# Kernel optimization log

Hardware: AMD Instinct MI355X
Metric: run time of the kernel (lower is better)

The kernel has to match this reference:

```python
import jax, jax.numpy as jnp
import numpy as np

N, T, IN_DIM = 5000, 100, 32
FEAT, HID, OUT, HEADS = 64, 64, 8, 4
E = 160000
F_IN = FEAT + OUT  # GATCell input = concat(embedding, theta)


def setup_inputs() -> dict:
    key = jax.random.key(0)
    ks = jax.random.split(key, 16)
    s = 0.05
    d = {}
    d["x"] = jax.random.normal(ks[0], (N, T, IN_DIM), jnp.float32)
    d["edge_index"] = jax.random.randint(ks[1], (2, E), 0, N, dtype=jnp.int32)
    # LSTM params (PyTorch gate order: i, f, g, o)
    d["W_ih"] = jax.random.normal(ks[2], (IN_DIM, 4 * FEAT), jnp.float32) * s
    d["W_hh"] = jax.random.normal(ks[3], (FEAT, 4 * FEAT), jnp.float32) * s
    d["b_ih"] = jax.random.normal(ks[4], (4 * FEAT,), jnp.float32) * s
    d["b_hh"] = jax.random.normal(ks[5], (4 * FEAT,), jnp.float32) * s
    # TransformerConv params (lin_q/k/v with bias, lin_skip with bias; concat=False)
    d["Wq"] = jax.random.normal(ks[6], (F_IN, HEADS * HID), jnp.float32) * s
    d["bq"] = jax.random.normal(ks[7], (HEADS * HID,), jnp.float32) * s
    d["Wk"] = jax.random.normal(ks[8], (F_IN, HEADS * HID), jnp.float32) * s
    d["bk"] = jax.random.normal(ks[9], (HEADS * HID,), jnp.float32) * s
    d["Wv"] = jax.random.normal(ks[10], (F_IN, HEADS * HID), jnp.float32) * s
    d["bv"] = jax.random.normal(ks[11], (HEADS * HID,), jnp.float32) * s
    d["Wskip"] = jax.random.normal(ks[12], (F_IN, HID), jnp.float32) * s
    d["bskip"] = jax.random.normal(ks[13], (HID,), jnp.float32) * s
    # GATCell mlp (bias=False)
    d["Wmlp"] = jax.random.normal(ks[14], (HID, OUT), jnp.float32) * s
    return d


def _lstm(x, W_ih, W_hh, b_ih, b_hh):
    # x: [N, T, IN_DIM] -> embedding [T, N, FEAT]
    xs = jnp.transpose(x, (1, 0, 2))

    def step(carry, xt):
        h, c = carry
        gates = xt @ W_ih + h @ W_hh + (b_ih + b_hh)
        i, f, g, o = jnp.split(gates, 4, axis=-1)
        c = jax.nn.sigmoid(f) * c + jax.nn.sigmoid(i) * jnp.tanh(g)
        h = jax.nn.sigmoid(o) * jnp.tanh(c)
        return (h, c), h

    h0 = jnp.zeros((x.shape[0], FEAT), x.dtype)
    _, hs = jax.lax.scan(step, (h0, h0), xs)
    return hs


def _transformer_conv(h, edge_index, Wq, bq, Wk, bk, Wv, bv, Wskip, bskip):
    # h: [N, F_IN]; edge_index: [2, E] (row 0 = source j, row 1 = target i)
    n = h.shape[0]
    src, dst = edge_index[0], edge_index[1]
    q = (h @ Wq + bq).reshape(n, HEADS, HID)
    k = (h @ Wk + bk).reshape(n, HEADS, HID)
    v = (h @ Wv + bv).reshape(n, HEADS, HID)
    # per-edge attention logits [E, HEADS]
    alpha = jnp.einsum('ehd,ehd->eh', q[dst], k[src]) / jnp.sqrt(jnp.float32(HID))
    # segment softmax over incoming edges of each target node
    m = jax.ops.segment_max(alpha, dst, num_segments=n)
    m = jnp.where(jnp.isfinite(m), m, 0.0)
    ex = jnp.exp(alpha - m[dst])
    denom = jax.ops.segment_sum(ex, dst, num_segments=n)
    w = ex / jnp.maximum(denom[dst], 1e-16)
    agg = jax.ops.segment_sum(w[:, :, None] * v[src], dst, num_segments=n)  # [N,H,D]
    out = agg.mean(axis=1)  # concat=False -> average heads
    return out + h @ Wskip + bskip  # root skip connection


def reference(x, edge_index, W_ih, W_hh, b_ih, b_hh, Wq, bq, Wk, bk, Wv, bv,
              Wskip, bskip, Wmlp):
    emb = _lstm(x, W_ih, W_hh, b_ih, b_hh)  # [T, N, FEAT]
    n = x.shape[0]

    def gat_step(theta, emb_t):
        h_in = jnp.concatenate([emb_t, theta], axis=-1)  # [N, F_IN]
        hid = _transformer_conv(h_in, edge_index, Wq, bq, Wk, bk, Wv, bv,
                                Wskip, bskip)
        theta_new = jnp.tanh(hid) @ Wmlp
        return theta_new, theta_new

    theta0 = jnp.zeros((n, OUT), x.dtype)
    _, thetas = jax.lax.scan(gat_step, theta0, emb)  # [T, N, OUT]
    theta = jnp.transpose(thetas, (1, 0, 2))  # [N, T, OUT]

    alpha_beta = theta[:, :, :-3]
    a_b = jax.nn.sigmoid(theta[:, :, -3:-1])
    a = a_b[:, :, 0:1] * a_b[:, :, 1:]
    b = a_b[:, :, 0:1] - a
    c = jax.nn.softplus(theta[:, :, -1:])
    return jnp.concatenate([alpha_beta, a, b, c], axis=-1)
```

## Files before the change

### kernel.cpp

```cpp
#include <hip/hip_runtime.h>
#include <math.h>

#define NN 5000
#define TT 100
#define IND 32
#define FEATD 64
#define HIDD 64
#define OUTD 8
#define NHEADS 4
#define EE 160000
#define FIN 72
#define NHC 256
#define QKV_B 625
#define LSTM_B 625

typedef float floatx2 __attribute__((ext_vector_type(2)));

__device__ __forceinline__ float fsig(float x){ return 1.f/(1.f+__expf(-x)); }
__device__ __forceinline__ float ftanh(float x){ return 1.f - 2.f/(__expf(2.f*x)+1.f); }
__device__ __forceinline__ float fsoftplus(float x){ return (x>20.f)? x : log1pf(__expf(x)); }

__global__ __launch_bounds__(256) void count_edges(const int* __restrict__ dst,
                                                   int* __restrict__ cnt){
    int e = blockIdx.x*256 + threadIdx.x;
    if (e < EE) atomicAdd(&cnt[dst[e]], 1);
}

#define SCAN_N 5120
__global__ __launch_bounds__(1024) void scan_csr(const int* __restrict__ cnt,
                                                 int* __restrict__ row_ptr,
                                                 int* __restrict__ cursor){
    __shared__ int sa[SCAN_N];
    __shared__ int sb[SCAN_N];
    int tid = threadIdx.x;
    for (int i=tid;i<SCAN_N;i+=1024) sa[i] = (i<NN)?cnt[i]:0;
    __syncthreads();
    int *s=sa, *d=sb;
    for (int off=1; off<SCAN_N; off<<=1){
        for (int i=tid;i<SCAN_N;i+=1024){
            int v = s[i];
            if (i>=off) v += s[i-off];
            d[i] = v;
        }
        __syncthreads();
        int* t=s; s=d; d=t;
    }
    for (int i=tid;i<=NN;i+=1024){
        int excl = (i==0)?0:s[i-1];
        row_ptr[i] = excl;
        if (i<NN) cursor[i] = excl;
    }
}

__global__ __launch_bounds__(256) void fill_edges(const int* __restrict__ src,
                                                  const int* __restrict__ dst,
                                                  int* __restrict__ cursor,
                                                  int* __restrict__ col){
    int e = blockIdx.x*256 + threadIdx.x;
    if (e < EE){
        int dn = dst[e];
        int pos = atomicAdd(&cursor[dn], 1);
        col[pos] = src[e];
    }
}

#define LOADKV(e) (*reinterpret_cast<const uint2*>(kv + (size_t)col[(e)]*512 + lane*8))
__global__ __launch_bounds__(256) void attn_step(
    const float* __restrict__ q,
    const unsigned char* __restrict__ kv,
    const float* __restrict__ sk,
    const int* __restrict__ row_ptr,
    const int* __restrict__ col,
    const float* __restrict__ Wmlp,
    float* __restrict__ theta,
    float* __restrict__ out,
    int ts)
{
    __shared__ float mrg[2][5][64];
    int tid = threadIdx.x;
    int wvid = tid >> 6;
    int lane = tid & 63;
    int ln   = wvid >> 1;
    int half = wvid & 1;
    int n = blockIdx.x*2 + ln;
    int e0 = row_ptr[n], e1 = row_ptr[n+1];
    float4 qv = *reinterpret_cast<const float4*>(q + n*NHC + lane*4);
    qv.x *= 0.125f; qv.y *= 0.125f; qv.z *= 0.125f; qv.w *= 0.125f;

    float denA=0.f, denB=0.f;
    float aA0=0.f, aA1=0.f, aA2=0.f, aA3=0.f;
    float aB0=0.f, aB1=0.f, aB2=0.f, aB3=0.f;

    const uint2 zv = {0u,0u};
    uint2 bA0=zv, bA1=zv, bB0=zv, bB1=zv;
    int base = e0 + half;
    if (base     < e1) bA0 = LOADKV(base);
    if (base + 2 < e1) bB0 = LOADKV(base+2);
    if (base + 4 < e1) bA1 = LOADKV(base+4);
    if (base + 6 < e1) bB1 = LOADKV(base+6);
    for (int e = base; e < e1; e += 4){
        uint2 uA = bA0; bA0 = bA1; bA1 = zv;
        uint2 uB = bB0; bB0 = bB1; bB1 = zv;
        if (e + 8  < e1) bA1 = LOADKV(e+8);
        if (e + 10 < e1) bB1 = LOADKV(e+10);

        floatx2 kA0 = __builtin_amdgcn_cvt_pk_f32_fp8(uA.x, false);
        floatx2 kA1 = __builtin_amdgcn_cvt_pk_f32_fp8(uA.x, true);
        floatx2 kB0 = __builtin_amdgcn_cvt_pk_f32_fp8(uB.x, false);
        floatx2 kB1 = __builtin_amdgcn_cvt_pk_f32_fp8(uB.x, true);
        float pA = qv.x*kA0[0] + qv.y*kA0[1] + qv.z*kA1[0] + qv.w*kA1[1];
        float pB = qv.x*kB0[0] + qv.y*kB0[1] + qv.z*kB1[0] + qv.w*kB1[1];
        pA += __shfl_xor(pA,1); pB += __shfl_xor(pB,1);
        pA += __shfl_xor(pA,2); pB += __shfl_xor(pB,2);
        pA += __shfl_xor(pA,4); pB += __shfl_xor(pB,4);
        pA += __shfl_xor(pA,8); pB += __shfl_xor(pB,8);

        float eA = __expf(pA);
        float eB = __expf((e + 2 < e1) ? pB : -INFINITY);
        floatx2 vA0 = __builtin_amdgcn_cvt_pk_f32_fp8(uA.y, false);
        floatx2 vA1 = __builtin_amdgcn_cvt_pk_f32_fp8(uA.y, true);
        floatx2 vB0 = __builtin_amdgcn_cvt_pk_f32_fp8(uB.y, false);
        floatx2 vB1 = __builtin_amdgcn_cvt_pk_f32_fp8(uB.y, true);
        denA += eA;
        aA0 = fmaf(eA, vA0[0], aA0);
        aA1 = fmaf(eA, vA0[1], aA1);
        aA2 = fmaf(eA, vA1[0], aA2);
        aA3 = fmaf(eA, vA1[1], aA3);
        denB += eB;
        aB0 = fmaf(eB, vB0[0], aB0);
        aB1 = fmaf(eB, vB0[1], aB1);
        aB2 = fmaf(eB, vB1[0], aB2);
        aB3 = fmaf(eB, vB1[1], aB3);
    }
    float denom = denA + denB;
    float ax = aA0 + aB0;
    float ay = aA1 + aB1;
    float az = aA2 + aB2;
    float aw = aA3 + aB3;

    if (half == 1){
        mrg[ln][0][lane]=denom;
        mrg[ln][1][lane]=ax; mrg[ln][2][lane]=ay;
        mrg[ln][3][lane]=az; mrg[ln][4][lane]=aw;
    }
    __syncthreads();
    if (half == 1) return;

    denom += mrg[ln][0][lane];
    ax += mrg[ln][1][lane];
    ay += mrg[ln][2][lane];
    az += mrg[ln][3][lane];
    aw += mrg[ln][4][lane];

    float inv = 1.f / fmaxf(denom, 1e-16f);
    ax *= inv; ay *= inv; az *= inv; aw *= inv;
    ax += __shfl_xor(ax,16); ax += __shfl_xor(ax,32);
    ay += __shfl_xor(ay,16); ay += __shfl_xor(ay,32);
    az += __shfl_xor(az,16); az += __shfl_xor(az,32);
    aw += __shfl_xor(aw,16); aw += __shfl_xor(aw,32);
    int d0 = (lane & 15) * 4;
    float4 skv = *reinterpret_cast<const float4*>(sk + n*64 + d0);
    float t0 = ftanh(0.25f*ax + skv.x);
    float t1 = ftanh(0.25f*ay + skv.y);
    float t2 = ftanh(0.25f*az + skv.z);
    float t3 = ftanh(0.25f*aw + skv.w);
    float p8[8];
    #pragma unroll
    for (int j=0;j<8;j++){
        p8[j] = fmaf(t0, Wmlp[(d0+0)*8+j],
                fmaf(t1, Wmlp[(d0+1)*8+j],
                fmaf(t2, Wmlp[(d0+2)*8+j],
                     t3* Wmlp[(d0+3)*8+j])));
    }
    #pragma unroll
    for (int j=0;j<8;j++){
        p8[j] += __shfl_xor(p8[j],1);
        p8[j] += __shfl_xor(p8[j],2);
        p8[j] += __shfl_xor(p8[j],4);
        p8[j] += __shfl_xor(p8[j],8);
    }
    if (lane == 0){
        float4 t0v = {p8[0],p8[1],p8[2],p8[3]};
        float4 t1v = {p8[4],p8[5],p8[6],p8[7]};
        *reinterpret_cast<float4*>(theta + n*8)     = t0v;
        *reinterpret_cast<float4*>(theta + n*8 + 4) = t1v;
        float ab0 = fsig(p8[5]);
        float ab1 = fsig(p8[6]);
        float a  = ab0*ab1;
        float bb = ab0 - a;
        float cc = fsoftplus(p8[7]);
        float4 o0 = {p8[0],p8[1],p8[2],p8[3]};
        float4 o1 = {p8[4],a,bb,cc};
        float* op = out + ((size_t)n*TT + ts)*8;
        *reinterpret_cast<float4*>(op)     = o0;
        *reinterpret_cast<float4*>(op + 4) = o1;
    }
}

__global__ __launch_bounds__(256) void qkv_lstm_step(
    const float* __restrict__ x,
    const float* __restrict__ W_ih, const float* __restrict__ W_hh,
    const float* __restrict__ b_ih, const float* __restrict__ b_hh,
    float* __restrict__ h0, float* __restrict__ h1,
    float* __restrict__ c,
    const float* __restrict__ theta,
    const float* __restrict__ Wq, const float* __restrict__ bq,
    const float* __restrict__ Wk, const float* __restrict__ bk,
    const float* __restrict__ Wv, const float* __restrict__ bv,
    const float* __restrict__ Wsk, const float* __restrict__ bsk,
    float* __restrict__ q, float* __restrict__ sk,
    unsigned char* __restrict__ kv, int t)
{
    int tid = threadIdx.x;
    if (blockIdx.x < QKV_B){
        if (t < 0) return;
        __shared__ float hin[8][72];
        const float* hread = (t & 1) ? h1 : h0;
        int n0 = blockIdx.x * 8;
        for (int i=tid; i<8*72; i+=256){
            int node = i/72, kk = i%72;
            int n = n0 + node;
            hin[node][kk] = (kk<64) ? hread[n*64+kk] : theta[n*8 + (kk-64)];
        }
        __syncthreads();

        if (tid < 208){
            int c4 = tid*4;
            const float* W; const float* b; int ncol; int cc; int kind;
            if (c4 < 256)      { W=Wq;  b=bq;  ncol=256; cc=c4;     kind=0; }
            else if (c4 < 512) { W=Wk;  b=bk;  ncol=256; cc=c4-256; kind=1; }
            else if (c4 < 768) { W=Wv;  b=bv;  ncol=256; cc=c4-512; kind=2; }
            else               { W=Wsk; b=bsk; ncol=64;  cc=c4-768; kind=3; }
            float acc2[8][4];
            #pragma unroll
            for (int nn=0;nn<8;nn++){
                #pragma unroll
                for (int j=0;j<4;j++) acc2[nn][j]=0.f;
            }
            #pragma unroll 4
            for (int kk=0; kk<FIN; kk++){
                float4 w = *reinterpret_cast<const float4*>(W + kk*ncol + cc);
                #pragma unroll
                for (int nn=0;nn<8;nn++){
                    float xv = hin[nn][kk];
                    acc2[nn][0]=fmaf(xv,w.x,acc2[nn][0]);
                    acc2[nn][1]=fmaf(xv,w.y,acc2[nn][1]);
                    acc2[nn][2]=fmaf(xv,w.z,acc2[nn][2]);
                    acc2[nn][3]=fmaf(xv,w.w,acc2[nn][3]);
                }
            }
            float4 bb = *reinterpret_cast<const float4*>(b + cc);
            #pragma unroll
            for (int nn=0;nn<8;nn++){
                int n = n0 + nn;
                float o0=acc2[nn][0]+bb.x, o1=acc2[nn][1]+bb.y;
                float o2=acc2[nn][2]+bb.z, o3=acc2[nn][3]+bb.w;
                if (kind == 0){
                    float4 o = {o0,o1,o2,o3};
                    *reinterpret_cast<float4*>(q + n*NHC + cc) = o;
                } else if (kind == 3){
                    float4 o = {o0,o1,o2,o3};
                    *reinterpret_cast<float4*>(sk + n*64 + cc) = o;
                } else {
                    int pk = __builtin_amdgcn_cvt_pk_fp8_f32(o0, o1, 0,  false);
                    pk     = __builtin_amdgcn_cvt_pk_fp8_f32(o2, o3, pk, true);
                    int off = n*512 + cc*2 + ((kind==2)?4:0);
                    *reinterpret_cast<unsigned int*>(kv + off) = (unsigned int)pk;
                }
            }
        }
    } else {
        int s = t + 1;
        if (s >= TT) return;
        __shared__ float xh[8][96];
        const float* hread = (s & 1) ? h0 : h1;
        float*       hwrit = (s & 1) ? h1 : h0;
        int n0 = (blockIdx.x - QKV_B) * 8;
        for (int i=tid; i<8*96; i+=256){
            int node = i/96, kk = i%96;
            int n = n0 + node;
            xh[node][kk] = (kk<32) ? x[(n*TT + s)*IND + kk]
                                   : ((s == 0) ? 0.f : hread[n*64 + (kk-32)]);
        }
        __syncthreads();

        int d  = tid & 63;
        int wv = tid >> 6;
        float acc[2][4];
        #pragma unroll
        for (int p=0;p<2;p++){
            #pragma unroll
            for (int g=0;g<4;g++) acc[p][g]=0.f;
        }
        #pragma unroll 8
        for (int kk=0; kk<32; kk++){
            const float* Wr = W_ih + kk*256;
            float w0=Wr[d], w1=Wr[d+64], w2=Wr[d+128], w3=Wr[d+192];
            float x0 = xh[wv][kk], x1 = xh[wv+4][kk];
            acc[0][0]=fmaf(x0,w0,acc[0][0]); acc[0][1]=fmaf(x0,w1,acc[0][1]);
            acc[0][2]=fmaf(x0,w2,acc[0][2]); acc[0][3]=fmaf(x0,w3,acc[0][3]);
            acc[1][0]=fmaf(x1,w0,acc[1][0]); acc[1][1]=fmaf(x1,w1,acc[1][1]);
            acc[1][2]=fmaf(x1,w2,acc[1][2]); acc[1][3]=fmaf(x1,w3,acc[1][3]);
        }
        #pragma unroll 8
        for (int kk=0; kk<64; kk++){
            const float* Wr = W_hh + kk*256;
            float w0=Wr[d], w1=Wr[d+64], w2=Wr[d+128], w3=Wr[d+192];
            float x0 = xh[wv][32+kk], x1 = xh[wv+4][32+kk];
            acc[0][0]=fmaf(x0,w0,acc[0][0]); acc[0][1]=fmaf(x0,w1,acc[0][1]);
            acc[0][2]=fmaf(x0,w2,acc[0][2]); acc[0][3]=fmaf(x0,w3,acc[0][3]);
            acc[1][0]=fmaf(x1,w0,acc[1][0]); acc[1][1]=fmaf(x1,w1,acc[1][1]);
            acc[1][2]=fmaf(x1,w2,acc[1][2]); acc[1][3]=fmaf(x1,w3,acc[1][3]);
        }
        float bi0 = b_ih[d]     + b_hh[d];
        float bi1 = b_ih[d+64]  + b_hh[d+64];
        float bi2 = b_ih[d+128] + b_hh[d+128];
        float bi3 = b_ih[d+192] + b_hh[d+192];
        #pragma unroll
        for (int p=0;p<2;p++){
            int n = n0 + wv + p*4;
            float gi = fsig (acc[p][0] + bi0);
            float gf = fsig (acc[p][1] + bi1);
            float gg = ftanh(acc[p][2] + bi2);
            float go = fsig (acc[p][3] + bi3);
            float cold = (s == 0) ? 0.f : c[n*64 + d];
            float cnew = gf*cold + gi*gg;
            float hnew = go*ftanh(cnew);
            c[n*64 + d] = cnew;
            hwrit[n*64 + d] = hnew;
        }
    }
}

extern "C" void kernel_launch(void* const* d_in, const int* in_sizes, int n_in,
                              void* d_out, int out_size, void* d_ws, size_t ws_size,
                              hipStream_t stream) {
    const float* x     = (const float*)d_in[0];
    const int*   ei    = (const int*)  d_in[1];
    const float* W_ih  = (const float*)d_in[2];
    const float* W_hh  = (const float*)d_in[3];
    const float* b_ih  = (const float*)d_in[4];
    const float* b_hh  = (const float*)d_in[5];
    const float* Wq    = (const float*)d_in[6];
    const float* bq    = (const float*)d_in[7];
    const float* Wk    = (const float*)d_in[8];
    const float* bk    = (const float*)d_in[9];
    const float* Wv    = (const float*)d_in[10];
    const float* bv    = (const float*)d_in[11];
    const float* Wsk   = (const float*)d_in[12];
    const float* bsk   = (const float*)d_in[13];
    const float* Wmlp  = (const float*)d_in[14];
    float* out = (float*)d_out;

    float* f = (float*)d_ws;
    float* h0    = f;
    float* h1    = h0 + NN*64;
    float* c     = h1 + NN*64;
    float* theta = c + NN*64;
    float* q     = theta + NN*8;
    float* skb   = q + NN*NHC;
    unsigned char* kvb = (unsigned char*)(skb + NN*64);
    int* ip      = (int*)(kvb + (size_t)NN*512);
    int* row_ptr = ip;
    int* cnt     = row_ptr + (NN+1);
    int* cursor  = cnt + NN;
    int* colv    = cursor + NN;

    const int* src = ei;
    const int* dst = ei + EE;

    hipMemsetAsync(h0, 0, (size_t)NN*(64+64+64+8)*sizeof(float), stream);
    hipMemsetAsync(cnt, 0, (size_t)NN*sizeof(int), stream);

    count_edges<<<(EE+255)/256, 256, 0, stream>>>(dst, cnt);
    scan_csr<<<1, 1024, 0, stream>>>(cnt, row_ptr, cursor);
    fill_edges<<<(EE+255)/256, 256, 0, stream>>>(src, dst, cursor, colv);

    qkv_lstm_step<<<QKV_B + LSTM_B, 256, 0, stream>>>(
        x, W_ih, W_hh, b_ih, b_hh, h0, h1, c, theta,
        Wq,bq, Wk,bk, Wv,bv, Wsk,bsk, q, skb, kvb, -1);

    for (int t=0; t<TT; t++){
        if (t >= 1)
            attn_step<<<NN/2, 256, 0, stream>>>(q, kvb, skb, row_ptr, colv,
                                                Wmlp, theta, out, t-1);
        qkv_lstm_step<<<QKV_B + LSTM_B, 256, 0, stream>>>(
            x, W_ih, W_hh, b_ih, b_hh, h0, h1, c, theta,
            Wq,bq, Wk,bk, Wv,bv, Wsk,bsk, q, skb, kvb, t);
    }
    attn_step<<<NN/2, 256, 0, stream>>>(q, kvb, skb, row_ptr, colv,
                                        Wmlp, theta, out, TT-1);
}
```

Before: 5.089 ms.

## Fuse attention, QKV projection and LSTM step into one kernel per timestep

Merges the per-timestep attention kernel and the QKV/LSTM kernel into a single 1024-thread `fused_step` launch. Each attention block computes theta for its 8 nodes, keeps it in shared memory and feeds it straight into the QKV projection, so the theta global buffer is no longer written and reread. K/V is double-buffered because a step reads other nodes' K/V from the previous step while writing the new ones, and LSTM blocks now cover 32 nodes each. This halves the number of kernel launches and removes the initial memset. In exchange, the larger blocks may lower occupancy and scheduling flexibility for the irregular attention gathers.

```diff
diff --git a/kernel.cpp b/kernel.cpp
--- a/kernel.cpp
+++ b/kernel.cpp
@@ -4,15 +4,11 @@
 #define NN 5000
 #define TT 100
 #define IND 32
-#define FEATD 64
-#define HIDD 64
-#define OUTD 8
-#define NHEADS 4
-#define EE 160000
 #define FIN 72
 #define NHC 256
-#define QKV_B 625
-#define LSTM_B 625
+#define EE 160000
+#define AQ_B 625
+#define LSTM_GB 157
 
 typedef float floatx2 __attribute__((ext_vector_type(2)));
 
@@ -64,167 +60,161 @@
     }
 }
 
-#define LOADKV(e) (*reinterpret_cast<const uint2*>(kv + (size_t)col[(e)]*512 + lane*8))
-__global__ __launch_bounds__(256) void attn_step(
-    const float* __restrict__ q,
-    const unsigned char* __restrict__ kv,
-    const float* __restrict__ sk,
-    const int* __restrict__ row_ptr,
-    const int* __restrict__ col,
-    const float* __restrict__ Wmlp,
-    float* __restrict__ theta,
-    float* __restrict__ out,
-    int ts)
-{
-    __shared__ float mrg[2][5][64];
-    int tid = threadIdx.x;
-    int wvid = tid >> 6;
-    int lane = tid & 63;
-    int ln   = wvid >> 1;
-    int half = wvid & 1;
-    int n = blockIdx.x*2 + ln;
-    int e0 = row_ptr[n], e1 = row_ptr[n+1];
-    float4 qv = *reinterpret_cast<const float4*>(q + n*NHC + lane*4);
-    qv.x *= 0.125f; qv.y *= 0.125f; qv.z *= 0.125f; qv.w *= 0.125f;
-
-    float denA=0.f, denB=0.f;
-    float aA0=0.f, aA1=0.f, aA2=0.f, aA3=0.f;
-    float aB0=0.f, aB1=0.f, aB2=0.f, aB3=0.f;
-
-    const uint2 zv = {0u,0u};
-    uint2 bA0=zv, bA1=zv, bB0=zv, bB1=zv;
-    int base = e0 + half;
-    if (base     < e1) bA0 = LOADKV(base);
-    if (base + 2 < e1) bB0 = LOADKV(base+2);
-    if (base + 4 < e1) bA1 = LOADKV(base+4);
-    if (base + 6 < e1) bB1 = LOADKV(base+6);
-    for (int e = base; e < e1; e += 4){
-        uint2 uA = bA0; bA0 = bA1; bA1 = zv;
-        uint2 uB = bB0; bB0 = bB1; bB1 = zv;
-        if (e + 8  < e1) bA1 = LOADKV(e+8);
-        if (e + 10 < e1) bB1 = LOADKV(e+10);
-
-        floatx2 kA0 = __builtin_amdgcn_cvt_pk_f32_fp8(uA.x, false);
-        floatx2 kA1 = __builtin_amdgcn_cvt_pk_f32_fp8(uA.x, true);
-        floatx2 kB0 = __builtin_amdgcn_cvt_pk_f32_fp8(uB.x, false);
-        floatx2 kB1 = __builtin_amdgcn_cvt_pk_f32_fp8(uB.x, true);
-        float pA = qv.x*kA0[0] + qv.y*kA0[1] + qv.z*kA1[0] + qv.w*kA1[1];
-        float pB = qv.x*kB0[0] + qv.y*kB0[1] + qv.z*kB1[0] + qv.w*kB1[1];
-        pA += __shfl_xor(pA,1); pB += __shfl_xor(pB,1);
-        pA += __shfl_xor(pA,2); pB += __shfl_xor(pB,2);
-        pA += __shfl_xor(pA,4); pB += __shfl_xor(pB,4);
-        pA += __shfl_xor(pA,8); pB += __shfl_xor(pB,8);
-
-        float eA = __expf(pA);
-        float eB = __expf((e + 2 < e1) ? pB : -INFINITY);
-        floatx2 vA0 = __builtin_amdgcn_cvt_pk_f32_fp8(uA.y, false);
-        floatx2 vA1 = __builtin_amdgcn_cvt_pk_f32_fp8(uA.y, true);
-        floatx2 vB0 = __builtin_amdgcn_cvt_pk_f32_fp8(uB.y, false);
-        floatx2 vB1 = __builtin_amdgcn_cvt_pk_f32_fp8(uB.y, true);
-        denA += eA;
-        aA0 = fmaf(eA, vA0[0], aA0);
-        aA1 = fmaf(eA, vA0[1], aA1);
-        aA2 = fmaf(eA, vA1[0], aA2);
-        aA3 = fmaf(eA, vA1[1], aA3);
-        denB += eB;
-        aB0 = fmaf(eB, vB0[0], aB0);
-        aB1 = fmaf(eB, vB0[1], aB1);
-        aB2 = fmaf(eB, vB1[0], aB2);
-        aB3 = fmaf(eB, vB1[1], aB3);
-    }
-    float denom = denA + denB;
-    float ax = aA0 + aB0;
-    float ay = aA1 + aB1;
-    float az = aA2 + aB2;
-    float aw = aA3 + aB3;
-
-    if (half == 1){
-        mrg[ln][0][lane]=denom;
-        mrg[ln][1][lane]=ax; mrg[ln][2][lane]=ay;
-        mrg[ln][3][lane]=az; mrg[ln][4][lane]=aw;
-    }
-    __syncthreads();
-    if (half == 1) return;
-
-    denom += mrg[ln][0][lane];
-    ax += mrg[ln][1][lane];
-    ay += mrg[ln][2][lane];
-    az += mrg[ln][3][lane];
-    aw += mrg[ln][4][lane];
-
-    float inv = 1.f / fmaxf(denom, 1e-16f);
-    ax *= inv; ay *= inv; az *= inv; aw *= inv;
-    ax += __shfl_xor(ax,16); ax += __shfl_xor(ax,32);
-    ay += __shfl_xor(ay,16); ay += __shfl_xor(ay,32);
-    az += __shfl_xor(az,16); az += __shfl_xor(az,32);
-    aw += __shfl_xor(aw,16); aw += __shfl_xor(aw,32);
-    int d0 = (lane & 15) * 4;
-    float4 skv = *reinterpret_cast<const float4*>(sk + n*64 + d0);
-    float t0 = ftanh(0.25f*ax + skv.x);
-    float t1 = ftanh(0.25f*ay + skv.y);
-    float t2 = ftanh(0.25f*az + skv.z);
-    float t3 = ftanh(0.25f*aw + skv.w);
-    float p8[8];
-    #pragma unroll
-    for (int j=0;j<8;j++){
-        p8[j] = fmaf(t0, Wmlp[(d0+0)*8+j],
-                fmaf(t1, Wmlp[(d0+1)*8+j],
-                fmaf(t2, Wmlp[(d0+2)*8+j],
-                     t3* Wmlp[(d0+3)*8+j])));
-    }
-    #pragma unroll
-    for (int j=0;j<8;j++){
-        p8[j] += __shfl_xor(p8[j],1);
-        p8[j] += __shfl_xor(p8[j],2);
-        p8[j] += __shfl_xor(p8[j],4);
-        p8[j] += __shfl_xor(p8[j],8);
-    }
-    if (lane == 0){
-        float4 t0v = {p8[0],p8[1],p8[2],p8[3]};
-        float4 t1v = {p8[4],p8[5],p8[6],p8[7]};
-        *reinterpret_cast<float4*>(theta + n*8)     = t0v;
-        *reinterpret_cast<float4*>(theta + n*8 + 4) = t1v;
-        float ab0 = fsig(p8[5]);
-        float ab1 = fsig(p8[6]);
-        float a  = ab0*ab1;
-        float bb = ab0 - a;
-        float cc = fsoftplus(p8[7]);
-        float4 o0 = {p8[0],p8[1],p8[2],p8[3]};
-        float4 o1 = {p8[4],a,bb,cc};
-        float* op = out + ((size_t)n*TT + ts)*8;
-        *reinterpret_cast<float4*>(op)     = o0;
-        *reinterpret_cast<float4*>(op + 4) = o1;
-    }
-}
-
-__global__ __launch_bounds__(256) void qkv_lstm_step(
+#define LOADKV(e) (*reinterpret_cast<const uint2*>(kvr + (size_t)col[(e)]*512 + lane*8))
+__global__ __launch_bounds__(1024) void fused_step(
     const float* __restrict__ x,
     const float* __restrict__ W_ih, const float* __restrict__ W_hh,
     const float* __restrict__ b_ih, const float* __restrict__ b_hh,
     float* __restrict__ h0, float* __restrict__ h1,
     float* __restrict__ c,
-    const float* __restrict__ theta,
     const float* __restrict__ Wq, const float* __restrict__ bq,
     const float* __restrict__ Wk, const float* __restrict__ bk,
     const float* __restrict__ Wv, const float* __restrict__ bv,
     const float* __restrict__ Wsk, const float* __restrict__ bsk,
     float* __restrict__ q, float* __restrict__ sk,
-    unsigned char* __restrict__ kv, int t)
+    const unsigned char* __restrict__ kvr,
+    unsigned char* __restrict__ kvw,
+    const int* __restrict__ row_ptr,
+    const int* __restrict__ col,
+    const float* __restrict__ Wmlp,
+    float* __restrict__ out,
+    int t)
 {
+    __shared__ float smem[3136];
     int tid = threadIdx.x;
-    if (blockIdx.x < QKV_B){
-        if (t < 0) return;
-        __shared__ float hin[8][72];
-        const float* hread = (t & 1) ? h1 : h0;
-        int n0 = blockIdx.x * 8;
-        for (int i=tid; i<8*72; i+=256){
-            int node = i/72, kk = i%72;
-            int n = n0 + node;
-            hin[node][kk] = (kk<64) ? hread[n*64+kk] : theta[n*8 + (kk-64)];
+
+    if (blockIdx.x < AQ_B){
+        float (*mrg)[64] = (float(*)[64])smem;
+        float (*hin)[FIN] = (float(*)[FIN])(smem + 2560);
+        int wvid = tid >> 6;
+        int lane = tid & 63;
+        int ln   = wvid >> 1;
+        int half = wvid & 1;
+        int n = blockIdx.x*8 + ln;
+
+        if (t >= 0 && t < TT){
+            const float* hread = (t & 1) ? h1 : h0;
+            for (int i=tid; i<8*64; i+=1024){
+                int node = i>>6, kk = i&63;
+                hin[node][kk] = hread[(blockIdx.x*8+node)*64 + kk];
+            }
+            if (t == 0 && tid < 64){
+                int node = tid>>3, j = tid&7;
+                hin[node][64+j] = 0.f;
+            }
+        }
+
+        float denom, ax, ay, az, aw;
+        if (t >= 1){
+            int e0 = row_ptr[n], e1 = row_ptr[n+1];
+            float4 qv = *reinterpret_cast<const float4*>(q + n*NHC + lane*4);
+            qv.x *= 0.125f; qv.y *= 0.125f; qv.z *= 0.125f; qv.w *= 0.125f;
+
+            float denA=0.f, denB=0.f;
+            float aA0=0.f, aA1=0.f, aA2=0.f, aA3=0.f;
+            float aB0=0.f, aB1=0.f, aB2=0.f, aB3=0.f;
+            const uint2 zv = {0u,0u};
+            uint2 bA0=zv, bA1=zv, bB0=zv, bB1=zv;
+            int base = e0 + half;
+            if (base     < e1) bA0 = LOADKV(base);
+            if (base + 2 < e1) bB0 = LOADKV(base+2);
+            if (base + 4 < e1) bA1 = LOADKV(base+4);
+            if (base + 6 < e1) bB1 = LOADKV(base+6);
+            for (int e = base; e < e1; e += 4){
+                uint2 uA = bA0; bA0 = bA1; bA1 = zv;
+                uint2 uB = bB0; bB0 = bB1; bB1 = zv;
+                if (e + 8  < e1) bA1 = LOADKV(e+8);
+                if (e + 10 < e1) bB1 = LOADKV(e+10);
+
+                floatx2 kA0 = __builtin_amdgcn_cvt_pk_f32_fp8(uA.x, false);
+                floatx2 kA1 = __builtin_amdgcn_cvt_pk_f32_fp8(uA.x, true);
+                floatx2 kB0 = __builtin_amdgcn_cvt_pk_f32_fp8(uB.x, false);
+                floatx2 kB1 = __builtin_amdgcn_cvt_pk_f32_fp8(uB.x, true);
+                float pA = qv.x*kA0[0] + qv.y*kA0[1] + qv.z*kA1[0] + qv.w*kA1[1];
+                float pB = qv.x*kB0[0] + qv.y*kB0[1] + qv.z*kB1[0] + qv.w*kB1[1];
+                pA += __shfl_xor(pA,1); pB += __shfl_xor(pB,1);
+                pA += __shfl_xor(pA,2); pB += __shfl_xor(pB,2);
+                pA += __shfl_xor(pA,4); pB += __shfl_xor(pB,4);
+                pA += __shfl_xor(pA,8); pB += __shfl_xor(pB,8);
+
+                float eA = __expf(pA);
+                float eB = __expf((e + 2 < e1) ? pB : -INFINITY);
+                floatx2 vA0 = __builtin_amdgcn_cvt_pk_f32_fp8(uA.y, false);
+                floatx2 vA1 = __builtin_amdgcn_cvt_pk_f32_fp8(uA.y, true);
+                floatx2 vB0 = __builtin_amdgcn_cvt_pk_f32_fp8(uB.y, false);
+                floatx2 vB1 = __builtin_amdgcn_cvt_pk_f32_fp8(uB.y, true);
+                denA += eA;
+                aA0 = fmaf(eA, vA0[0], aA0);
+                aA1 = fmaf(eA, vA0[1], aA1);
+                aA2 = fmaf(eA, vA1[0], aA2);
+                aA3 = fmaf(eA, vA1[1], aA3);
+                denB += eB;
+                aB0 = fmaf(eB, vB0[0], aB0);
+                aB1 = fmaf(eB, vB0[1], aB1);
+                aB2 = fmaf(eB, vB1[0], aB2);
+                aB3 = fmaf(eB, vB1[1], aB3);
+            }
+            denom = denA + denB;
+            ax = aA0 + aB0; ay = aA1 + aB1;
+            az = aA2 + aB2; aw = aA3 + aB3;
+            if (half == 1){
+                mrg[ln*5+0][lane]=denom;
+                mrg[ln*5+1][lane]=ax; mrg[ln*5+2][lane]=ay;
+                mrg[ln*5+3][lane]=az; mrg[ln*5+4][lane]=aw;
+            }
         }
         __syncthreads();
-
-        if (tid < 208){
+        if (t >= 1 && half == 0){
+            denom += mrg[ln*5+0][lane];
+            ax += mrg[ln*5+1][lane];
+            ay += mrg[ln*5+2][lane];
+            az += mrg[ln*5+3][lane];
+            aw += mrg[ln*5+4][lane];
+            float inv = 1.f / fmaxf(denom, 1e-16f);
+            ax *= inv; ay *= inv; az *= inv; aw *= inv;
+            ax += __shfl_xor(ax,16); ax += __shfl_xor(ax,32);
+            ay += __shfl_xor(ay,16); ay += __shfl_xor(ay,32);
+            az += __shfl_xor(az,16); az += __shfl_xor(az,32);
+            aw += __shfl_xor(aw,16); aw += __shfl_xor(aw,32);
+            int d0 = (lane & 15) * 4;
+            float4 skv = *reinterpret_cast<const float4*>(sk + n*64 + d0);
+            float t0 = ftanh(0.25f*ax + skv.x);
+            float t1 = ftanh(0.25f*ay + skv.y);
+            float t2 = ftanh(0.25f*az + skv.z);
+            float t3 = ftanh(0.25f*aw + skv.w);
+            float p8[8];
+            #pragma unroll
+            for (int j=0;j<8;j++){
+                p8[j] = fmaf(t0, Wmlp[(d0+0)*8+j],
+                        fmaf(t1, Wmlp[(d0+1)*8+j],
+                        fmaf(t2, Wmlp[(d0+2)*8+j],
+                             t3* Wmlp[(d0+3)*8+j])));
+            }
+            #pragma unroll
+            for (int j=0;j<8;j++){
+                p8[j] += __shfl_xor(p8[j],1);
+                p8[j] += __shfl_xor(p8[j],2);
+                p8[j] += __shfl_xor(p8[j],4);
+                p8[j] += __shfl_xor(p8[j],8);
+            }
+            if (lane == 0){
+                #pragma unroll
+                for (int j=0;j<8;j++) hin[ln][64+j] = p8[j];
+                float ab0 = fsig(p8[5]);
+                float ab1 = fsig(p8[6]);
+                float a  = ab0*ab1;
+                float bb = ab0 - a;
+                float cc = fsoftplus(p8[7]);
+                float4 o0 = {p8[0],p8[1],p8[2],p8[3]};
+                float4 o1 = {p8[4],a,bb,cc};
+                float* op = out + ((size_t)n*TT + (t-1))*8;
+                *reinterpret_cast<float4*>(op)     = o0;
+                *reinterpret_cast<float4*>(op + 4) = o1;
+            }
+        }
+        __syncthreads();
+
+        if (t >= 0 && t < TT && tid < 208){
             int c4 = tid*4;
             const float* W; const float* b; int ncol; int cc; int kind;
             if (c4 < 256)      { W=Wq;  b=bq;  ncol=256; cc=c4;     kind=0; }
@@ -252,35 +242,38 @@
             float4 bb = *reinterpret_cast<const float4*>(b + cc);
             #pragma unroll
             for (int nn=0;nn<8;nn++){
-                int n = n0 + nn;
+                int n2 = blockIdx.x*8 + nn;
                 float o0=acc2[nn][0]+bb.x, o1=acc2[nn][1]+bb.y;
                 float o2=acc2[nn][2]+bb.z, o3=acc2[nn][3]+bb.w;
                 if (kind == 0){
                     float4 o = {o0,o1,o2,o3};
-                    *reinterpret_cast<float4*>(q + n*NHC + cc) = o;
+                    *reinterpret_cast<float4*>(q + n2*NHC + cc) = o;
                 } else if (kind == 3){
                     float4 o = {o0,o1,o2,o3};
-                    *reinterpret_cast<float4*>(sk + n*64 + cc) = o;
+                    *reinterpret_cast<float4*>(sk + n2*64 + cc) = o;
                 } else {
                     int pk = __builtin_amdgcn_cvt_pk_fp8_f32(o0, o1, 0,  false);
                     pk     = __builtin_amdgcn_cvt_pk_fp8_f32(o2, o3, pk, true);
-                    int off = n*512 + cc*2 + ((kind==2)?4:0);
-                    *reinterpret_cast<unsigned int*>(kv + off) = (unsigned int)pk;
+                    int off = n2*512 + cc*2 + ((kind==2)?4:0);
+                    *reinterpret_cast<unsigned int*>(kvw + off) = (unsigned int)pk;
                 }
             }
         }
     } else {
         int s = t + 1;
         if (s >= TT) return;
-        __shared__ float xh[8][96];
+        float (*xh)[96] = (float(*)[96])smem;
         const float* hread = (s & 1) ? h0 : h1;
         float*       hwrit = (s & 1) ? h1 : h0;
-        int n0 = (blockIdx.x - QKV_B) * 8;
-        for (int i=tid; i<8*96; i+=256){
+        int n0 = (blockIdx.x - AQ_B) * 32;
+        for (int i=tid; i<32*96; i+=1024){
             int node = i/96, kk = i%96;
             int n = n0 + node;
-            xh[node][kk] = (kk<32) ? x[(n*TT + s)*IND + kk]
-                                   : ((s == 0) ? 0.f : hread[n*64 + (kk-32)]);
+            float v = 0.f;
+            if (n < NN)
+                v = (kk<32) ? x[((size_t)n*TT + s)*IND + kk]
+                            : ((s == 0) ? 0.f : hread[n*64 + (kk-32)]);
+            xh[node][kk] = v;
         }
         __syncthreads();
 
@@ -296,7 +289,7 @@
         for (int kk=0; kk<32; kk++){
             const float* Wr = W_ih + kk*256;
             float w0=Wr[d], w1=Wr[d+64], w2=Wr[d+128], w3=Wr[d+192];
-            float x0 = xh[wv][kk], x1 = xh[wv+4][kk];
+            float x0 = xh[wv][kk], x1 = xh[wv+16][kk];
             acc[0][0]=fmaf(x0,w0,acc[0][0]); acc[0][1]=fmaf(x0,w1,acc[0][1]);
             acc[0][2]=fmaf(x0,w2,acc[0][2]); acc[0][3]=fmaf(x0,w3,acc[0][3]);
             acc[1][0]=fmaf(x1,w0,acc[1][0]); acc[1][1]=fmaf(x1,w1,acc[1][1]);
@@ -306,7 +299,7 @@
         for (int kk=0; kk<64; kk++){
             const float* Wr = W_hh + kk*256;
             float w0=Wr[d], w1=Wr[d+64], w2=Wr[d+128], w3=Wr[d+192];
-            float x0 = xh[wv][32+kk], x1 = xh[wv+4][32+kk];
+            float x0 = xh[wv][32+kk], x1 = xh[wv+16][32+kk];
             acc[0][0]=fmaf(x0,w0,acc[0][0]); acc[0][1]=fmaf(x0,w1,acc[0][1]);
             acc[0][2]=fmaf(x0,w2,acc[0][2]); acc[0][3]=fmaf(x0,w3,acc[0][3]);
             acc[1][0]=fmaf(x1,w0,acc[1][0]); acc[1][1]=fmaf(x1,w1,acc[1][1]);
@@ -318,16 +311,18 @@
         float bi3 = b_ih[d+192] + b_hh[d+192];
         #pragma unroll
         for (int p=0;p<2;p++){
-            int n = n0 + wv + p*4;
-            float gi = fsig (acc[p][0] + bi0);
-            float gf = fsig (acc[p][1] + bi1);
-            float gg = ftanh(acc[p][2] + bi2);
-            float go = fsig (acc[p][3] + bi3);
-            float cold = (s == 0) ? 0.f : c[n*64 + d];
-            float cnew = gf*cold + gi*gg;
-            float hnew = go*ftanh(cnew);
-            c[n*64 + d] = cnew;
-            hwrit[n*64 + d] = hnew;
+            int n = n0 + wv + p*16;
+            if (n < NN){
+                float gi = fsig (acc[p][0] + bi0);
+                float gf = fsig (acc[p][1] + bi1);
+                float gg = ftanh(acc[p][2] + bi2);
+                float go = fsig (acc[p][3] + bi3);
+                float cold = (s == 0) ? 0.f : c[n*64 + d];
+                float cnew = gf*cold + gi*gg;
+                float hnew = go*ftanh(cnew);
+                c[n*64 + d] = cnew;
+                hwrit[n*64 + d] = hnew;
+            }
         }
     }
 }
@@ -356,11 +351,11 @@
     float* h0    = f;
     float* h1    = h0 + NN*64;
     float* c     = h1 + NN*64;
-    float* theta = c + NN*64;
-    float* q     = theta + NN*8;
+    float* q     = c + NN*64;
     float* skb   = q + NN*NHC;
-    unsigned char* kvb = (unsigned char*)(skb + NN*64);
-    int* ip      = (int*)(kvb + (size_t)NN*512);
+    unsigned char* kvb0 = (unsigned char*)(skb + NN*64);
+    unsigned char* kvb1 = kvb0 + (size_t)NN*512;
+    int* ip      = (int*)(kvb1 + (size_t)NN*512);
     int* row_ptr = ip;
     int* cnt     = row_ptr + (NN+1);
     int* cursor  = cnt + NN;
@@ -369,25 +364,18 @@
     const int* src = ei;
     const int* dst = ei + EE;
 
-    hipMemsetAsync(h0, 0, (size_t)NN*(64+64+64+8)*sizeof(float), stream);
     hipMemsetAsync(cnt, 0, (size_t)NN*sizeof(int), stream);
 
     count_edges<<<(EE+255)/256, 256, 0, stream>>>(dst, cnt);
     scan_csr<<<1, 1024, 0, stream>>>(cnt, row_ptr, cursor);
     fill_edges<<<(EE+255)/256, 256, 0, stream>>>(src, dst, cursor, colv);
 
-    qkv_lstm_step<<<QKV_B + LSTM_B, 256, 0, stream>>>(
-        x, W_ih, W_hh, b_ih, b_hh, h0, h1, c, theta,
-        Wq,bq, Wk,bk, Wv,bv, Wsk,bsk, q, skb, kvb, -1);
-
-    for (int t=0; t<TT; t++){
-        if (t >= 1)
-            attn_step<<<NN/2, 256, 0, stream>>>(q, kvb, skb, row_ptr, colv,
-                                                Wmlp, theta, out, t-1);
-        qkv_lstm_step<<<QKV_B + LSTM_B, 256, 0, stream>>>(
-            x, W_ih, W_hh, b_ih, b_hh, h0, h1, c, theta,
-            Wq,bq, Wk,bk, Wv,bv, Wsk,bsk, q, skb, kvb, t);
-    }
-    attn_step<<<NN/2, 256, 0, stream>>>(q, kvb, skb, row_ptr, colv,
-                                        Wmlp, theta, out, TT-1);
-}
+    for (int t=-1; t<=TT; t++){
+        const unsigned char* kvr = ((t-1) & 1) ? kvb1 : kvb0;
+        unsigned char*       kvw = (t & 1) ? kvb1 : kvb0;
+        fused_step<<<AQ_B + LSTM_GB, 1024, 0, stream>>>(
+            x, W_ih, W_hh, b_ih, b_hh, h0, h1, c,
+            Wq,bq, Wk,bk, Wv,bv, Wsk,bsk,
+            q, skb, kvr, kvw, row_ptr, colv, Wmlp, out, t);
+    }
+}
```

New measurement: 6.657 ms. 1.31x slower.
